# Performance work log

Hardware: AMD Instinct MI355X
Metric: run time of the kernel (lower is better)

The kernel has to match this reference:

```python
import jax, jax.numpy as jnp
import numpy as np
import math

B, S, DIM = 4, 1024, 4096
N_HEADS, N_KV_HEADS = 32, 8
HEAD_DIM = DIM // N_HEADS  # 128
PAST = 1024
N_REP = N_HEADS // N_KV_HEADS


def _rope_freqs(seq_len, head_dim, theta=10000.0):
    inv = 1.0 / (theta ** (np.arange(0, head_dim, 2, dtype=np.float32) / head_dim))
    t = np.arange(seq_len, dtype=np.float32)
    ang = np.outer(t, inv)  # (S, head_dim//2)
    return jnp.asarray(np.cos(ang)), jnp.asarray(np.sin(ang))


def setup_inputs() -> dict:
    key = jax.random.key(0)
    ks = jax.random.split(key, 8)
    sc = 0.02
    x = jax.random.normal(ks[0], (B, S, DIM), dtype=jnp.float32)
    freqs_cos, freqs_sin = _rope_freqs(S, HEAD_DIM)
    cache_k = jax.random.normal(ks[1], (B, N_KV_HEADS, PAST, HEAD_DIM), dtype=jnp.float32)
    cache_v = jax.random.normal(ks[2], (B, N_KV_HEADS, PAST, HEAD_DIM), dtype=jnp.float32)
    wq = jax.random.normal(ks[3], (DIM, DIM), dtype=jnp.float32) * sc
    wk = jax.random.normal(ks[4], (N_KV_HEADS * HEAD_DIM, DIM), dtype=jnp.float32) * sc
    wv = jax.random.normal(ks[5], (N_KV_HEADS * HEAD_DIM, DIM), dtype=jnp.float32) * sc
    wo = jax.random.normal(ks[6], (DIM, DIM), dtype=jnp.float32) * sc
    return {"x": x, "freqs_cos": freqs_cos, "freqs_sin": freqs_sin,
            "cache_k": cache_k, "cache_v": cache_v,
            "wq": wq, "wk": wk, "wv": wv, "wo": wo}


def _apply_rotary(x, cos, sin):
    # x: (b, h, s, d); cos/sin: (s, d//2) broadcast to (1, 1, s, d//2)
    xr = x.reshape(*x.shape[:-1], -1, 2)
    x_r, x_i = xr[..., 0], xr[..., 1]
    cos = cos[None, None, :, :]
    sin = sin[None, None, :, :]
    out_r = x_r * cos - x_i * sin
    out_i = x_r * sin + x_i * cos
    return jnp.stack([out_r, out_i], axis=-1).reshape(x.shape)


def reference(x, freqs_cos, freqs_sin, cache_k, cache_v, wq, wk, wv, wo):
    bsz, seqlen, _ = x.shape
    xq = x @ wq.T  # (b, s, n_heads*hd)
    xk = x @ wk.T  # (b, s, n_kv*hd)
    xv = x @ wv.T
    xq = xq.reshape(bsz, seqlen, N_HEADS, HEAD_DIM).transpose(0, 2, 1, 3)
    xk = xk.reshape(bsz, seqlen, N_KV_HEADS, HEAD_DIM).transpose(0, 2, 1, 3)
    xv = xv.reshape(bsz, seqlen, N_KV_HEADS, HEAD_DIM).transpose(0, 2, 1, 3)
    xq = _apply_rotary(xq, freqs_cos, freqs_sin)
    xk = _apply_rotary(xk, freqs_cos, freqs_sin)
    keys = jnp.concatenate([cache_k, xk], axis=2)    # (b, kvh, past+s, hd)
    values = jnp.concatenate([cache_v, xv], axis=2)
    keys = jnp.repeat(keys, N_REP, axis=1)            # (b, h, kv, hd)
    values = jnp.repeat(values, N_REP, axis=1)
    scores = jnp.einsum('bhsd,bhkd->bhsk', xq, keys) / math.sqrt(HEAD_DIM)
    scores = jax.nn.softmax(scores, axis=-1)          # no mask (inference path)
    out = jnp.einsum('bhsk,bhkd->bhsd', scores, values)
    out = out.transpose(0, 2, 1, 3).reshape(bsz, seqlen, -1)
    return out @ wo.T
```

## Files before the change

### kernel.cpp

```cpp
#include <hip/hip_runtime.h>
#include <hip/hip_bf16.h>

using bf16 = __hip_bfloat16;
typedef __attribute__((ext_vector_type(4))) float f4;
typedef __attribute__((ext_vector_type(16))) float f16v;
typedef __attribute__((ext_vector_type(8))) short s8v;
typedef __attribute__((ext_vector_type(4))) short s4v;
typedef __attribute__((ext_vector_type(4))) unsigned int u4v;
typedef unsigned int u32;

__device__ __forceinline__ short f2bf(float x) {
  bf16 h = __float2bfloat16(x);
  return *reinterpret_cast<short*>(&h);
}

__device__ __forceinline__ u32 pkbf(float lo, float hi) {
  return (u32)(unsigned short)f2bf(lo) | ((u32)(unsigned short)f2bf(hi) << 16);
}

__device__ __forceinline__ void gload16(const bf16* g, bf16* l) {
  __builtin_amdgcn_global_load_lds(
      (const __attribute__((address_space(1))) u32*)g,
      (__attribute__((address_space(3))) u32*)l, 16, 0, 0);
}

__device__ __forceinline__ void swp32(u32& a, u32& b, int h) {
#if __has_builtin(__builtin_amdgcn_permlane32_swap)
  typedef __attribute__((ext_vector_type(2))) int i2v;
  i2v r = __builtin_amdgcn_permlane32_swap((int)a, (int)b, false, false);
  a = (u32)r.x;
  b = (u32)r.y;
#else
  u32 as = (u32)__shfl_xor((int)a, 32), bs = (u32)__shfl_xor((int)b, 32);
  u32 an = h ? bs : a, bn = h ? b : as;
  a = an;
  b = bn;
#endif
}

__global__ __launch_bounds__(256) void cvt_bf16(const float* __restrict__ src,
                                                bf16* __restrict__ dst) {
  size_t e = ((size_t)blockIdx.x * 256 + threadIdx.x) << 3;
  f4 a = *(const f4*)(src + e);
  f4 b = *(const f4*)(src + e + 4);
  s8v r = { f2bf(a[0]), f2bf(a[1]), f2bf(a[2]), f2bf(a[3]),
            f2bf(b[0]), f2bf(b[1]), f2bf(b[2]), f2bf(b[3]) };
  *(s8v*)(dst + e) = r;
}

__global__ __launch_bounds__(256) void cvt_cache_k(const float* __restrict__ src,
                                                   bf16* __restrict__ dst) {
  size_t e = ((size_t)blockIdx.x * 256 + threadIdx.x) << 2;
  f4 v = *(const f4*)(src + e);
  unsigned d = (unsigned)(e & 127u), p = (unsigned)((e >> 7) & 1023u), bk = (unsigned)(e >> 17);
  s4v r = { f2bf(v[0]), f2bf(v[1]), f2bf(v[2]), f2bf(v[3]) };
  *(s4v*)(dst + (((size_t)bk * 2048 + p) << 7) + d) = r;
}

__global__ __launch_bounds__(256) void cvt_cache_v(const float* __restrict__ src,
                                                   bf16* __restrict__ dst) {
  size_t e = ((size_t)blockIdx.x * 256 + threadIdx.x) << 2;
  unsigned p = (unsigned)(e & 1023u), d = (unsigned)((e >> 10) & 127u), bk = (unsigned)(e >> 17);
  const float* s = src + (((size_t)bk * 1024 + p) << 7) + d;
  s4v r = { f2bf(s[0]), f2bf(s[128]), f2bf(s[256]), f2bf(s[384]) };
  *(s4v*)(dst + (((size_t)bk * 128 + d) << 11) + p) = r;
}

__global__ __launch_bounds__(256) void rope_kernel(bf16* __restrict__ buf,
                                                   const float* __restrict__ fc,
                                                   const float* __restrict__ fs,
                                                   int sstride, int soff) {
  size_t t = (size_t)blockIdx.x * 256 + threadIdx.x;
  unsigned ip = (unsigned)(t & 63u);
  unsigned s  = (unsigned)((t >> 6) & 1023u);
  unsigned hh = (unsigned)(t >> 16);
  size_t base = ((size_t)hh * sstride + soff + s) * 128 + 2 * ip;
  unsigned u = *(unsigned*)(buf + base);
  float xr = __uint_as_float(u << 16);
  float xi = __uint_as_float(u & 0xffff0000u);
  float c = fc[s * 64 + ip], sn = fs[s * 64 + ip];
  unsigned short r0 = (unsigned short)f2bf(xr * c - xi * sn);
  unsigned short r1 = (unsigned short)f2bf(xr * sn + xi * c);
  *(unsigned*)(buf + base) = (unsigned)r0 | ((unsigned)r1 << 16);
}

#define MODE_Q   0
#define MODE_KV  1
#define MODE_OUT 2

template <int MODE>
__global__ __launch_bounds__(256) void gemm_bt(const bf16* __restrict__ A,
                                               const bf16* __restrict__ B,
                                               void* __restrict__ outp,
                                               void* __restrict__ outp2,
                                               int K, float scale) {
  __shared__ alignas(16) bf16 As[128 * 64];
  __shared__ alignas(16) bf16 Bs[128 * 64];

  const int tid = threadIdx.x;
  const int bm = blockIdx.x, bn = blockIdx.y;
  const int lane = tid & 63;
  const int wid = tid >> 6;
  const int wr = (wid >> 1) << 6;
  const int wc = (wid & 1) << 6;
  const int fr = lane & 15;
  const int g = lane >> 4;
  const int rg = g << 2;

  const int srow = tid >> 3;
  const int sc = (tid & 7) ^ (srow & 7);
  const bf16* aptr = A + (size_t)(bm * 128 + srow) * K + sc * 8;
  const bf16* bptr = B + (size_t)(bn * 128 + srow) * K + sc * 8;
  bf16* ldsA = &As[(size_t)((tid & 192) << 3)];
  bf16* ldsB = &Bs[(size_t)((tid & 192) << 3)];

  f4 acc[4][4] = {};

  const int nk = K >> 6;
  const size_t rstep = (size_t)32 * K;
  for (int kt = 0; kt < nk; ++kt) {
    const bf16* ak = aptr + kt * 64;
    const bf16* bk = bptr + kt * 64;
#pragma unroll
    for (int i = 0; i < 4; ++i) {
      gload16(ak + i * rstep, ldsA + i * 2048);
      gload16(bk + i * rstep, ldsB + i * 2048);
    }
    asm volatile("s_waitcnt vmcnt(0)" ::: "memory");
    __syncthreads();

#pragma unroll
    for (int ks = 0; ks < 2; ++ks) {
      s8v af[4], bfv[4];
      const int chc = (ks << 2) | g;
#pragma unroll
      for (int m = 0; m < 4; ++m) {
        const int row = wr + m * 16 + fr;
        af[m] = *(const s8v*)&As[row * 64 + ((chc ^ (row & 7)) << 3)];
      }
#pragma unroll
      for (int n = 0; n < 4; ++n) {
        const int row = wc + n * 16 + fr;
        bfv[n] = *(const s8v*)&Bs[row * 64 + ((chc ^ (row & 7)) << 3)];
      }
#pragma unroll
      for (int m = 0; m < 4; ++m)
#pragma unroll
        for (int n = 0; n < 4; ++n)
          acc[m][n] = __builtin_amdgcn_mfma_f32_16x16x32_bf16(af[m], bfv[n], acc[m][n], 0, 0, 0);
    }
    __syncthreads();
  }

#pragma unroll
  for (int m = 0; m < 4; ++m) {
    const int gr0 = bm * 128 + wr + m * 16 + rg;
    const int b = gr0 >> 10, s0 = gr0 & 1023;
#pragma unroll
    for (int n = 0; n < 4; ++n) {
      const int gcol = bn * 128 + wc + n * 16 + fr;
      if constexpr (MODE == MODE_OUT) {
#pragma unroll
        for (int j = 0; j < 4; ++j)
          ((float*)outp)[(size_t)(gr0 + j) * 4096 + gcol] = acc[m][n][j];
      } else if constexpr (MODE == MODE_Q) {
        const int h = gcol >> 7, d = gcol & 127;
#pragma unroll
        for (int j = 0; j < 4; ++j)
          ((bf16*)outp)[((((size_t)b * 32 + h) << 10) + s0 + j) * 128 + d] =
              __float2bfloat16(acc[m][n][j] * scale);
      } else {
        const int hv = (gcol >> 7) & 7, d = gcol & 127;
        if (gcol < 1024) {
#pragma unroll
          for (int j = 0; j < 4; ++j)
            ((bf16*)outp)[(((size_t)b * 8 + hv) * 2048 + 1024 + s0 + j) * 128 + d] =
                __float2bfloat16(acc[m][n][j]);
        } else {
          s4v r = { f2bf(acc[m][n][0]), f2bf(acc[m][n][1]),
                    f2bf(acc[m][n][2]), f2bf(acc[m][n][3]) };
          *(s4v*)((bf16*)outp2 + (((size_t)b * 8 + hv) * 128 + d) * 2048 + 1024 + s0) = r;
        }
      }
    }
  }
}

__global__ __launch_bounds__(512) void attn_kernel(const bf16* __restrict__ Q,
                                                   const bf16* __restrict__ Kf,
                                                   const bf16* __restrict__ Vt,
                                                   bf16* __restrict__ O) {
  __shared__ alignas(16) bf16 Kls[2][8192];
  __shared__ alignas(16) bf16 Vls[2][8192];

  const int tid = threadIdx.x;
  const int lane = tid & 63;
  const int w = tid >> 6;
  const int h = lane >> 5;
  const int q31 = lane & 31;
  const int rx = q31 & 7;

  const int qb = blockIdx.x;
  const int bh = blockIdx.y;
  const int b = bh >> 5, hd = bh & 31;
  const int kv = hd >> 2;

  const size_t qbase = (((size_t)b * 32 + hd) << 10) * 128;
  const size_t kbase = (((size_t)b * 8 + kv) * 2048) * 128;
  const size_t vbase = (((size_t)b * 8 + kv) * 128) * 2048;

  const int qrow = qb * 256 + w * 32 + q31;
  s8v qf[8];
#pragma unroll
  for (int c = 0; c < 8; ++c)
    qf[c] = *(const s8v*)&Q[qbase + (size_t)qrow * 128 + c * 16 + h * 8];

  const int sr = tid >> 3;
  const int swz8 = (((tid & 7) ^ (sr & 7)) << 3);
  const int wbase = w * 512;

  f16v oacc[4] = {};
  float mrun = -3e38f, lrun = 0.f;

  auto stage = [&](int kb, int bufi) {
    const bf16* ksrc = Kf + kbase + (size_t)(kb * 64 + sr) * 128 + swz8;
    gload16(ksrc,      &Kls[bufi][wbase]);
    gload16(ksrc + 64, &Kls[bufi][4096 + wbase]);
    const bf16* vsrc = Vt + vbase + (size_t)sr * 2048 + kb * 64 + swz8;
    gload16(vsrc,                      &Vls[bufi][wbase]);
    gload16(vsrc + (size_t)64 * 2048,  &Vls[bufi][4096 + wbase]);
  };

  stage(0, 0);
  asm volatile("s_waitcnt vmcnt(0)" ::: "memory");
  __syncthreads();

  for (int kb = 0; kb < 32; ++kb) {
    const int bufi = kb & 1;
    if (kb + 1 < 32) stage(kb + 1, bufi ^ 1);

    const bf16* KB = Kls[bufi];
    const bf16* VB = Vls[bufi];

    f16v sac[2] = {};
    __builtin_amdgcn_s_setprio(1);
#pragma unroll
    for (int c = 0; c < 8; ++c) {
      const int cc = 2 * c + h;
      const int cof = (cc >> 3) * 4096 + (((cc & 7) ^ rx) << 3);
      s8v k0 = *(const s8v*)&KB[cof + q31 * 64];
      s8v k1 = *(const s8v*)&KB[cof + (32 + q31) * 64];
      sac[0] = __builtin_amdgcn_mfma_f32_32x32x16_bf16(k0, qf[c], sac[0], 0, 0, 0);
      sac[1] = __builtin_amdgcn_mfma_f32_32x32x16_bf16(k1, qf[c], sac[1], 0, 0, 0);
    }
    __builtin_amdgcn_s_setprio(0);

    float pm = -3e38f;
#pragma unroll
    for (int r = 0; r < 16; ++r) {
      pm = fmaxf(pm, sac[0][r]);
      pm = fmaxf(pm, sac[1][r]);
    }
    pm = fmaxf(pm, __shfl_xor(pm, 32));

    const bool skip = __all(pm <= mrun + 8.0f);
    if (!skip) {
      const float mnew = fmaxf(mrun, pm);
      const float corr = exp2f(mrun - mnew);
      mrun = mnew;
      lrun *= corr;
#pragma unroll
      for (int m = 0; m < 4; ++m)
#pragma unroll
        for (int r = 0; r < 16; ++r) oacc[m][r] *= corr;
    }
    float ls = 0.f;
#pragma unroll
    for (int s = 0; s < 2; ++s)
#pragma unroll
      for (int r = 0; r < 16; ++r) {
        const float p = exp2f(sac[s][r] - mrun);
        sac[s][r] = p;
        ls += p;
      }
    ls += __shfl_xor(ls, 32);
    lrun += ls;

    s8v F[4];
#pragma unroll
    for (int s = 0; s < 2; ++s) {
      u32 W[8];
#pragma unroll
      for (int t = 0; t < 8; ++t) W[t] = pkbf(sac[s][2 * t], sac[s][2 * t + 1]);
      swp32(W[0], W[2], h); swp32(W[1], W[3], h);
      swp32(W[4], W[6], h); swp32(W[5], W[7], h);
      union { u32 u[4]; s8v v; } f0, f1;
      f0.u[0] = W[0]; f0.u[1] = W[1]; f0.u[2] = W[2]; f0.u[3] = W[3];
      f1.u[0] = W[4]; f1.u[1] = W[5]; f1.u[2] = W[6]; f1.u[3] = W[7];
      F[s * 2] = f0.v;
      F[s * 2 + 1] = f1.v;
    }

    __builtin_amdgcn_s_setprio(1);
#pragma unroll
    for (int ksg = 0; ksg < 4; ++ksg) {
      const int cc2 = 2 * ksg + h;
      const int vof = ((cc2 ^ rx) << 3);
#pragma unroll
      for (int m = 0; m < 4; ++m) {
        s8v vf = *(const s8v*)&VB[(m * 32 + q31) * 64 + vof];
        oacc[m] = __builtin_amdgcn_mfma_f32_32x32x16_bf16(vf, F[ksg], oacc[m], 0, 0, 0);
      }
    }
    __builtin_amdgcn_s_setprio(0);

    asm volatile("s_waitcnt vmcnt(0)" ::: "memory");
    __syncthreads();
  }

  const float inv = 1.f / lrun;
  bf16* orow = O + ((size_t)b * 1024 + qrow) * 4096 + hd * 128;
#pragma unroll
  for (int m = 0; m < 4; ++m)
#pragma unroll
    for (int r = 0; r < 16; r += 2) {
      const int d = m * 32 + (r & 3) + 8 * (r >> 2) + 4 * h;
      *(u32*)&orow[d] = pkbf(oacc[m][r] * inv, oacc[m][r + 1] * inv);
    }
}

extern "C" void kernel_launch(void* const* d_in, const int* in_sizes, int n_in,
                              void* d_out, int out_size, void* d_ws, size_t ws_size,
                              hipStream_t stream) {
  const float* x  = (const float*)d_in[0];
  const float* fc = (const float*)d_in[1];
  const float* fs = (const float*)d_in[2];
  const float* ck = (const float*)d_in[3];
  const float* cv = (const float*)d_in[4];
  const float* wq = (const float*)d_in[5];
  const float* wk = (const float*)d_in[6];
  const float* wv = (const float*)d_in[7];
  const float* wo = (const float*)d_in[8];
  float* out = (float*)d_out;

  char* ws = (char*)d_ws;
  bf16* qr    = (bf16*)(ws);
  bf16* kfull = (bf16*)(ws + (32u << 20));
  bf16* vt    = (bf16*)(ws + (48u << 20));
  bf16* xb    = (bf16*)(ws + (64u << 20));
  bf16* attn  = xb;
  bf16* wqb   = (bf16*)(ws + (96u << 20));
  bf16* wob   = wqb;
  bf16* wkvb  = (bf16*)(ws + (128u << 20));

  cvt_bf16<<<8192, 256, 0, stream>>>(x, xb);
  cvt_bf16<<<8192, 256, 0, stream>>>(wq, wqb);
  cvt_bf16<<<2048, 256, 0, stream>>>(wk, wkvb);
  cvt_bf16<<<2048, 256, 0, stream>>>(wv, wkvb + 4194304);
  cvt_cache_k<<<4096, 256, 0, stream>>>(ck, kfull);
  cvt_cache_v<<<4096, 256, 0, stream>>>(cv, vt);

  gemm_bt<MODE_Q><<<dim3(32, 32), 256, 0, stream>>>(
      xb, wqb, qr, nullptr, 4096, 0.1275174198520337f);
  gemm_bt<MODE_KV><<<dim3(32, 16), 256, 0, stream>>>(
      xb, wkvb, kfull, vt, 4096, 1.0f);

  cvt_bf16<<<8192, 256, 0, stream>>>(wo, wob);

  rope_kernel<<<32768, 256, 0, stream>>>(qr, fc, fs, 1024, 0);
  rope_kernel<<<8192, 256, 0, stream>>>(kfull, fc, fs, 2048, 1024);

  attn_kernel<<<dim3(4, 128), 512, 0, stream>>>(qr, kfull, vt, attn);

  gemm_bt<MODE_OUT><<<dim3(32, 32), 256, 0, stream>>>(
      attn, wob, out, nullptr, 4096, 1.0f);
}
```

Baseline: 755.7 us.

## Fuse QKV projections into one double-buffered 256x256-tile GEMM with XCD swizzle

Replaces the 128x128 single-buffered GEMM with a 512-thread, 256x256-tile kernel. It double-buffers LDS and interleaves global-to-LDS prefetch of the next K tile with MFMA phases, using explicit barriers and priority hints. The Q, K and V projections are fused into one launch by treating the contiguous wq/wk/wv bf16 buffers as a single 6144-row B matrix. Block indices are remapped across the 8 XCDs. The intent is to raise data reuse and overlap loads with compute, at the cost of 128KB LDS per block and higher register pressure. The attention kernel's cross-half reductions now use permlane32 swap instead of shuffles.

```diff
diff --git a/kernel.cpp b/kernel.cpp
--- a/kernel.cpp
+++ b/kernel.cpp
@@ -35,6 +35,27 @@
   u32 an = h ? bs : a, bn = h ? b : as;
   a = an;
   b = bn;
+#endif
+}
+
+__device__ __forceinline__ float xhalf_max(float x) {
+#if __has_builtin(__builtin_amdgcn_permlane32_swap)
+  typedef __attribute__((ext_vector_type(2))) int i2v;
+  i2v r = __builtin_amdgcn_permlane32_swap(__float_as_int(x), __float_as_int(x),
+                                           false, false);
+  return fmaxf(__int_as_float(r.x), __int_as_float(r.y));
+#else
+  return fmaxf(x, __shfl_xor(x, 32));
+#endif
+}
+__device__ __forceinline__ float xhalf_sum(float x) {
+#if __has_builtin(__builtin_amdgcn_permlane32_swap)
+  typedef __attribute__((ext_vector_type(2))) int i2v;
+  i2v r = __builtin_amdgcn_permlane32_swap(__float_as_int(x), __float_as_int(x),
+                                           false, false);
+  return __int_as_float(r.x) + __int_as_float(r.y);
+#else
+  return x + __shfl_xor(x, 32);
 #endif
 }
 
@@ -84,102 +105,151 @@
   *(unsigned*)(buf + base) = (unsigned)r0 | ((unsigned)r1 << 16);
 }
 
-#define MODE_Q   0
-#define MODE_KV  1
-#define MODE_OUT 2
+#define MODE_QKV 0
+#define MODE_OUT 1
+
+#define PHASE_TAIL(AC, BC, KS, MH)                                           \
+  {                                                                          \
+    s8v af[4], bv[4];                                                        \
+    const int cofs = ((((KS) * 4) | g) ^ fx) << 3;                           \
+    _Pragma("unroll") for (int mi = 0; mi < 4; ++mi)                         \
+        af[mi] = *(const s8v*)&(AC)[aRowBase + ((MH)*4 + mi) * 1024 + cofs]; \
+    _Pragma("unroll") for (int ni = 0; ni < 4; ++ni)                         \
+        bv[ni] = *(const s8v*)&(BC)[bRowBase + ni * 1024 + cofs];            \
+    __builtin_amdgcn_s_barrier();                                            \
+    asm volatile("s_waitcnt lgkmcnt(0)" ::: "memory");                       \
+    __builtin_amdgcn_s_setprio(1);                                           \
+    _Pragma("unroll") for (int mi = 0; mi < 4; ++mi)                         \
+      _Pragma("unroll") for (int ni = 0; ni < 4; ++ni)                       \
+          acc[(MH)*4 + mi][ni] = __builtin_amdgcn_mfma_f32_16x16x32_bf16(    \
+              af[mi], bv[ni], acc[(MH)*4 + mi][ni], 0, 0, 0);                \
+    __builtin_amdgcn_s_setprio(0);                                           \
+    __builtin_amdgcn_s_barrier();                                            \
+  }
+
+#define PHASE_HEAD(AC, BC)                                                   \
+  {                                                                          \
+    __builtin_amdgcn_s_barrier();                                            \
+    s8v af[4], bv[4];                                                        \
+    const int cofs = (g ^ fx) << 3;                                          \
+    _Pragma("unroll") for (int mi = 0; mi < 4; ++mi)                         \
+        af[mi] = *(const s8v*)&(AC)[aRowBase + mi * 1024 + cofs];            \
+    _Pragma("unroll") for (int ni = 0; ni < 4; ++ni)                         \
+        bv[ni] = *(const s8v*)&(BC)[bRowBase + ni * 1024 + cofs];            \
+    asm volatile("s_waitcnt lgkmcnt(0)" ::: "memory");                       \
+    __builtin_amdgcn_s_setprio(1);                                           \
+    _Pragma("unroll") for (int mi = 0; mi < 4; ++mi)                         \
+      _Pragma("unroll") for (int ni = 0; ni < 4; ++ni)                       \
+          acc[mi][ni] = __builtin_amdgcn_mfma_f32_16x16x32_bf16(             \
+              af[mi], bv[ni], acc[mi][ni], 0, 0, 0);                         \
+    __builtin_amdgcn_s_setprio(0);                                           \
+    __builtin_amdgcn_s_barrier();                                            \
+  }
+
+#define KTILE(AC, BC, PA, PB, NA, NB, PF)                                    \
+  {                                                                          \
+    if (PF) { gload16((NA), (PA)); gload16((NA) + rstep, (PA) + 4096); }     \
+    if (PF) asm volatile("s_waitcnt vmcnt(2)" ::: "memory");                 \
+    else    asm volatile("s_waitcnt vmcnt(0)" ::: "memory");                 \
+    PHASE_HEAD(AC, BC)                                                       \
+    if (PF) { gload16((NA) + 2 * rstep, (PA) + 8192);                        \
+              gload16((NA) + 3 * rstep, (PA) + 12288); }                     \
+    PHASE_TAIL(AC, BC, 0, 1)                                                 \
+    if (PF) { gload16((NB), (PB)); gload16((NB) + rstep, (PB) + 4096); }     \
+    PHASE_TAIL(AC, BC, 1, 0)                                                 \
+    if (PF) { gload16((NB) + 2 * rstep, (PB) + 8192);                        \
+              gload16((NB) + 3 * rstep, (PB) + 12288); }                     \
+    PHASE_TAIL(AC, BC, 1, 1)                                                 \
+  }
 
 template <int MODE>
-__global__ __launch_bounds__(256) void gemm_bt(const bf16* __restrict__ A,
-                                               const bf16* __restrict__ B,
-                                               void* __restrict__ outp,
-                                               void* __restrict__ outp2,
-                                               int K, float scale) {
-  __shared__ alignas(16) bf16 As[128 * 64];
-  __shared__ alignas(16) bf16 Bs[128 * 64];
+__global__ __launch_bounds__(512, 2) void gemm256(const bf16* __restrict__ A,
+                                                  const bf16* __restrict__ B,
+                                                  void* __restrict__ o1,
+                                                  void* __restrict__ o2,
+                                                  void* __restrict__ o3,
+                                                  int K, float scale) {
+  extern __shared__ bf16 smem[];
+  bf16* A0 = smem;
+  bf16* A1 = smem + 16384;
+  bf16* B0 = smem + 32768;
+  bf16* B1 = smem + 49152;
 
   const int tid = threadIdx.x;
-  const int bm = blockIdx.x, bn = blockIdx.y;
   const int lane = tid & 63;
   const int wid = tid >> 6;
-  const int wr = (wid >> 1) << 6;
-  const int wc = (wid & 1) << 6;
+  const int wm = wid >> 2, wn = wid & 3;
   const int fr = lane & 15;
   const int g = lane >> 4;
   const int rg = g << 2;
-
-  const int srow = tid >> 3;
-  const int sc = (tid & 7) ^ (srow & 7);
-  const bf16* aptr = A + (size_t)(bm * 128 + srow) * K + sc * 8;
-  const bf16* bptr = B + (size_t)(bn * 128 + srow) * K + sc * 8;
-  bf16* ldsA = &As[(size_t)((tid & 192) << 3)];
-  bf16* ldsB = &Bs[(size_t)((tid & 192) << 3)];
-
-  f4 acc[4][4] = {};
+  const int fx = lane & 7;
+
+  const int gy = gridDim.y;
+  int lin = blockIdx.y * gridDim.x + blockIdx.x;
+  const int qq = (gridDim.x * gy) >> 3;
+  lin = (lin & 7) * qq + (lin >> 3);
+  const int bm = lin / gy;
+  const int bn = lin % gy;
+
+  const int r0 = tid >> 3;
+  const int sc = (tid & 7) ^ (r0 & 7);
+  const bf16* aptr = A + (size_t)(bm * 256 + r0) * K + sc * 8;
+  const bf16* bptr = B + (size_t)(bn * 256 + r0) * K + sc * 8;
+  const size_t rstep = (size_t)64 * K;
+  const int wofs = (tid & 448) << 3;
+  bf16* pA0 = A0 + wofs; bf16* pA1 = A1 + wofs;
+  bf16* pB0 = B0 + wofs; bf16* pB1 = B1 + wofs;
+
+  const int aRowBase = (wm * 128 + fr) * 64;
+  const int bRowBase = (wn * 64 + fr) * 64;
+
+  f4 acc[8][4] = {};
+
+#pragma unroll
+  for (int i = 0; i < 4; ++i) gload16(aptr + i * rstep, pA0 + i * 4096);
+#pragma unroll
+  for (int i = 0; i < 4; ++i) gload16(bptr + i * rstep, pB0 + i * 4096);
 
   const int nk = K >> 6;
-  const size_t rstep = (size_t)32 * K;
-  for (int kt = 0; kt < nk; ++kt) {
-    const bf16* ak = aptr + kt * 64;
-    const bf16* bk = bptr + kt * 64;
-#pragma unroll
-    for (int i = 0; i < 4; ++i) {
-      gload16(ak + i * rstep, ldsA + i * 2048);
-      gload16(bk + i * rstep, ldsB + i * 2048);
-    }
-    asm volatile("s_waitcnt vmcnt(0)" ::: "memory");
-    __syncthreads();
-
-#pragma unroll
-    for (int ks = 0; ks < 2; ++ks) {
-      s8v af[4], bfv[4];
-      const int chc = (ks << 2) | g;
-#pragma unroll
-      for (int m = 0; m < 4; ++m) {
-        const int row = wr + m * 16 + fr;
-        af[m] = *(const s8v*)&As[row * 64 + ((chc ^ (row & 7)) << 3)];
-      }
-#pragma unroll
-      for (int n = 0; n < 4; ++n) {
-        const int row = wc + n * 16 + fr;
-        bfv[n] = *(const s8v*)&Bs[row * 64 + ((chc ^ (row & 7)) << 3)];
-      }
-#pragma unroll
-      for (int m = 0; m < 4; ++m)
-#pragma unroll
-        for (int n = 0; n < 4; ++n)
-          acc[m][n] = __builtin_amdgcn_mfma_f32_16x16x32_bf16(af[m], bfv[n], acc[m][n], 0, 0, 0);
-    }
-    __syncthreads();
-  }
-
-#pragma unroll
-  for (int m = 0; m < 4; ++m) {
-    const int gr0 = bm * 128 + wr + m * 16 + rg;
-    const int b = gr0 >> 10, s0 = gr0 & 1023;
+  for (int kt = 0; kt < nk; kt += 2) {
+    const bf16* na = aptr + (kt + 1) * 64;
+    const bf16* nb = bptr + (kt + 1) * 64;
+    KTILE(A0, B0, pA1, pB1, na, nb, true)
+    const bool pf2 = (kt + 2 < nk);
+    const bf16* na2 = aptr + (kt + 2) * 64;
+    const bf16* nb2 = bptr + (kt + 2) * 64;
+    KTILE(A1, B1, pA0, pB0, na2, nb2, pf2)
+  }
+
+#pragma unroll
+  for (int m = 0; m < 8; ++m) {
+    const int grow0 = bm * 256 + wm * 128 + m * 16 + rg;
+    const int b = grow0 >> 10, s0 = grow0 & 1023;
 #pragma unroll
     for (int n = 0; n < 4; ++n) {
-      const int gcol = bn * 128 + wc + n * 16 + fr;
+      const int gcol = bn * 256 + wn * 64 + n * 16 + fr;
       if constexpr (MODE == MODE_OUT) {
 #pragma unroll
         for (int j = 0; j < 4; ++j)
-          ((float*)outp)[(size_t)(gr0 + j) * 4096 + gcol] = acc[m][n][j];
-      } else if constexpr (MODE == MODE_Q) {
-        const int h = gcol >> 7, d = gcol & 127;
-#pragma unroll
-        for (int j = 0; j < 4; ++j)
-          ((bf16*)outp)[((((size_t)b * 32 + h) << 10) + s0 + j) * 128 + d] =
-              __float2bfloat16(acc[m][n][j] * scale);
+          ((float*)o1)[(size_t)(grow0 + j) * 4096 + gcol] = acc[m][n][j];
       } else {
-        const int hv = (gcol >> 7) & 7, d = gcol & 127;
-        if (gcol < 1024) {
+        if (gcol < 4096) {
+          const int h = gcol >> 7, d = gcol & 127;
 #pragma unroll
           for (int j = 0; j < 4; ++j)
-            ((bf16*)outp)[(((size_t)b * 8 + hv) * 2048 + 1024 + s0 + j) * 128 + d] =
+            ((bf16*)o1)[((((size_t)b * 32 + h) << 10) + s0 + j) * 128 + d] =
+                __float2bfloat16(acc[m][n][j] * scale);
+        } else if (gcol < 5120) {
+          const int c = gcol - 4096, hv = c >> 7, d = c & 127;
+#pragma unroll
+          for (int j = 0; j < 4; ++j)
+            ((bf16*)o2)[(((size_t)b * 8 + hv) * 2048 + 1024 + s0 + j) * 128 + d] =
                 __float2bfloat16(acc[m][n][j]);
         } else {
+          const int c = gcol - 5120, hv = c >> 7, d = c & 127;
           s4v r = { f2bf(acc[m][n][0]), f2bf(acc[m][n][1]),
                     f2bf(acc[m][n][2]), f2bf(acc[m][n][3]) };
-          *(s4v*)((bf16*)outp2 + (((size_t)b * 8 + hv) * 128 + d) * 2048 + 1024 + s0) = r;
+          *(s4v*)((bf16*)o3 + (((size_t)b * 8 + hv) * 128 + d) * 2048 + 1024 + s0) = r;
         }
       }
     }
@@ -261,7 +331,7 @@
       pm = fmaxf(pm, sac[0][r]);
       pm = fmaxf(pm, sac[1][r]);
     }
-    pm = fmaxf(pm, __shfl_xor(pm, 32));
+    pm = xhalf_max(pm);
 
     const bool skip = __all(pm <= mrun + 8.0f);
     if (!skip) {
@@ -283,8 +353,7 @@
         sac[s][r] = p;
         ls += p;
       }
-    ls += __shfl_xor(ls, 32);
-    lrun += ls;
+    lrun += xhalf_sum(ls);
 
     s8v F[4];
 #pragma unroll
@@ -353,6 +422,11 @@
   bf16* wob   = wqb;
   bf16* wkvb  = (bf16*)(ws + (128u << 20));
 
+  hipFuncSetAttribute(reinterpret_cast<const void*>(&gemm256<MODE_QKV>),
+                      hipFuncAttributeMaxDynamicSharedMemorySize, 131072);
+  hipFuncSetAttribute(reinterpret_cast<const void*>(&gemm256<MODE_OUT>),
+                      hipFuncAttributeMaxDynamicSharedMemorySize, 131072);
+
   cvt_bf16<<<8192, 256, 0, stream>>>(x, xb);
   cvt_bf16<<<8192, 256, 0, stream>>>(wq, wqb);
   cvt_bf16<<<2048, 256, 0, stream>>>(wk, wkvb);
@@ -360,10 +434,8 @@
   cvt_cache_k<<<4096, 256, 0, stream>>>(ck, kfull);
   cvt_cache_v<<<4096, 256, 0, stream>>>(cv, vt);
 
-  gemm_bt<MODE_Q><<<dim3(32, 32), 256, 0, stream>>>(
-      xb, wqb, qr, nullptr, 4096, 0.1275174198520337f);
-  gemm_bt<MODE_KV><<<dim3(32, 16), 256, 0, stream>>>(
-      xb, wkvb, kfull, vt, 4096, 1.0f);
+  gemm256<MODE_QKV><<<dim3(16, 24), 512, 131072, stream>>>(
+      xb, wqb, qr, kfull, vt, 4096, 0.1275174198520337f);
 
   cvt_bf16<<<8192, 256, 0, stream>>>(wo, wob);
 
@@ -372,6 +444,6 @@
 
   attn_kernel<<<dim3(4, 128), 512, 0, stream>>>(qr, kfull, vt, attn);
 
-  gemm_bt<MODE_OUT><<<dim3(32, 32), 256, 0, stream>>>(
-      attn, wob, out, nullptr, 4096, 1.0f);
-}
+  gemm256<MODE_OUT><<<dim3(16, 16), 512, 131072, stream>>>(
+      attn, wob, out, nullptr, nullptr, 4096, 1.0f);
+}
```

Measured after the change: 667.5 us. 11.7% less time.
